# Performance work log

Measured on AMD Instinct MI355X. Metric: run time of the kernel, lower is better.

## Reference

```python
import jax, jax.numpy as jnp
import numpy as np


def _local_indices(H, W, K):
    # KxK local window per pixel; border neighbors clamped to the image (replicate padding)
    half = K // 2
    d = np.arange(-half, half + 1)
    r = np.clip(np.arange(H)[:, None, None, None] + d[None, None, :, None], 0, H - 1)
    c = np.clip(np.arange(W)[None, :, None, None] + d[None, None, None, :], 0, W - 1)
    return (r * W + c).reshape(H * W, K * K).astype(np.int32)


def setup_inputs():
    B, C, H, W = 2, 32, 128, 128
    K, S = 25, 1024
    N = H * W
    k1, k2, k3, k4 = jax.random.split(jax.random.key(0), 4)
    key_feat = jax.random.normal(k1, (B, C, H, W), dtype=jnp.float32)
    query_feat = jax.random.normal(k2, (B, C, H, W), dtype=jnp.float32)
    segment_target = jax.random.randint(k3, (B, 1, H, W), 0, 64, dtype=jnp.int32)
    local = jnp.broadcast_to(jnp.asarray(_local_indices(H, W, K))[None], (B, N, K * K))
    rand_glob = jax.random.randint(k4, (B, N, S - K * K), 0, N, dtype=jnp.int32)
    sample_inds = jnp.concatenate([local, rand_glob], axis=-1)  # [B, N, S]
    return {"key_feat": key_feat, "query_feat": query_feat,
            "segment_target": segment_target, "sample_inds": sample_inds}


def _affinity_logits(key_f, query_f, sample_inds, chunk=1024):
    # key_f, query_f: [B, N, C]; sample_inds: [B, N, S]
    B, N, C = key_f.shape
    S = sample_inds.shape[-1]
    nchunks = N // chunk
    q_c = query_f.reshape(B, nchunks, chunk, C).transpose(1, 0, 2, 3)
    i_c = sample_inds.reshape(B, nchunks, chunk, S).transpose(1, 0, 2, 3)

    def body(carry, args):
        q, idx = args                                   # [B, chunk, C], [B, chunk, S]
        kg = jax.vmap(lambda kb, ib: kb[ib])(key_f, idx)  # [B, chunk, S, C]
        return carry, jnp.einsum('bnsc,bnc->bns', kg, q)

    _, lc = jax.lax.scan(body, None, (q_c, i_c))        # [nchunks, B, chunk, S]
    logits = lc.transpose(1, 0, 2, 3).reshape(B, N, S)
    return logits * (C ** -0.5)


def _loss(logits, sample_inds, segment_target):
    B, N, S = logits.shape
    seg = segment_target.reshape(B, N)
    samples = jax.vmap(lambda s, i: s[i])(seg, sample_inds)      # [B, N, S]
    targets = (seg[:, :, None] == samples).astype(logits.dtype)
    mask = (seg != 0).astype(logits.dtype)[:, :, None]           # [B, N, 1]
    # weighted_softmax(logits, mask)
    xe = jnp.exp(logits - jnp.max(logits, -1, keepdims=True))
    denom = jnp.sum(xe * mask, -1, keepdims=True)
    y_prob = xe * mask / (denom + 1e-9)
    y_pred = jnp.log(jnp.clip(y_prob, 1e-8, None))
    y_true = targets / (jnp.sum(targets, -1, keepdims=True) + 1e-9)
    # F.kl_div(y_pred, y_true, reduction='none') with 0*log(0) = 0
    kl = jnp.where(y_true > 0,
                   y_true * (jnp.log(jnp.clip(y_true, 1e-30, None)) - y_pred),
                   0.0) * mask
    agg_mask = (jnp.sum(mask, -1) > 0).astype(logits.dtype)
    return jnp.sum(kl) / (jnp.sum(agg_mask) + 1e-9)


def reference(key_feat, query_feat, segment_target, sample_inds):
    B, C, H, W = key_feat.shape
    N = H * W
    key_f = key_feat.reshape(B, C, N).transpose(0, 2, 1)    # [B, N, C]
    query_f = query_feat.reshape(B, C, N).transpose(0, 2, 1)
    logits = _affinity_logits(key_f, query_f, sample_inds)  # [B, N, S], scaled by C**-0.5
    loss = _loss(logits, sample_inds, segment_target)
    return (logits, loss)
```

## Files before the change

### kernel.cpp

```cpp
#include <hip/hip_runtime.h>
#include <stdint.h>

typedef _Float16 h2 __attribute__((ext_vector_type(2)));

static constexpr int CDIM = 32;
static constexpr int NPIX = 16384;
static constexpr int SSAM = 1024;
static constexpr int ROWS_PER_BLOCK = 16;

__device__ __forceinline__ uint16_t f2h(float f) {
    union { _Float16 h; uint16_t u; } c;
    c.h = (_Float16)f;
    return c.u;
}

template<int CTRL>
__device__ __forceinline__ float dpp_add(float x) {
    int y = __builtin_amdgcn_mov_dpp(__float_as_int(x), CTRL, 0xF, 0xF, true);
    return x + __int_as_float(y);
}

__device__ __forceinline__ float dot2(h2 a, h2 b, float c) {
    return __builtin_amdgcn_fdot2(a, b, c, false);
}

__global__ __launch_bounds__(256)
void zero_words(uint32_t* __restrict__ p, int nwords)
{
    int i = blockIdx.x * 256 + threadIdx.x;
    if (i < nwords) p[i] = 0;
}

__global__ __launch_bounds__(256)
void prep_kernel(const float* __restrict__ key_f,
                 const float* __restrict__ query_f,
                 uint8_t* __restrict__ key16,
                 uint8_t* __restrict__ q16,
                 int N, int rows, float scale)
{
    int gI = blockIdx.x * 256 + threadIdx.x;
    if (gI >= rows) return;
    int b = gI / N, n = gI - b * N;
    const size_t cb = (size_t)b * CDIM;

    uint32_t kp[16], qp[16];
#pragma unroll
    for (int c = 0; c < CDIM; c += 2) {
        float k0 = key_f[(cb + c) * N + n];
        float k1 = key_f[(cb + c + 1) * N + n];
        float q0 = query_f[(cb + c) * N + n] * scale;
        float q1 = query_f[(cb + c + 1) * N + n] * scale;
        kp[c >> 1] = (uint32_t)f2h(k0) | ((uint32_t)f2h(k1) << 16);
        qp[c >> 1] = (uint32_t)f2h(q0) | ((uint32_t)f2h(q1) << 16);
    }
    uint4* ko = (uint4*)(key16 + ((size_t)gI << 6));
    uint4* qo = (uint4*)(q16 + ((size_t)gI << 6));
#pragma unroll
    for (int j = 0; j < 4; ++j) {
        ko[j] = make_uint4(kp[4*j], kp[4*j+1], kp[4*j+2], kp[4*j+3]);
        qo[j] = make_uint4(qp[4*j], qp[4*j+1], qp[4*j+2], qp[4*j+3]);
    }
}

__global__ __launch_bounds__(256)
void segbit_build(const int* __restrict__ seg32,
                  uint32_t* __restrict__ segbit,
                  int N, int rows)
{
    int g = blockIdx.x * 256 + threadIdx.x;
    if (g >= rows) return;
    int b = g / N, n = g - b * N;
    int v = seg32[g] & 63;
    atomicOr(&segbit[(((size_t)(b * 64 + v)) << 9) + (n >> 5)], 1u << (n & 31));
}

__global__ __launch_bounds__(256)
void affinity_multi(const int* __restrict__ inds,
                    const uint8_t* __restrict__ key16,
                    const uint8_t* __restrict__ q16,
                    const int* __restrict__ seg32,
                    const uint32_t* __restrict__ segbit,
                    float* __restrict__ out,
                    float* __restrict__ ws_kl)
{
    const int tid  = threadIdx.x;
    const int row0 = blockIdx.x * ROWS_PER_BLOCK;
    const int b    = row0 >> 14;
    const int lane = tid & 63;
    const int w    = tid >> 6;
    const int g    = lane >> 2;
    const int sub  = lane & 3;

    __shared__ __align__(16) int      idx_lds[2][SSAM];
    __shared__ __align__(16) uint32_t bm_lds[2][512];
    __shared__ float red[2][3][4];

    const uint32_t* sbase_bm = segbit + ((size_t)(b * 64) << 9);

    ((int4*)idx_lds[0])[tid] = ((const int4*)(inds + ((size_t)row0 << 10)))[tid];
    int scur = seg32[row0];
    ((uint2*)bm_lds[0])[tid] =
        ((const uint2*)(sbase_bm + ((size_t)(scur & 63) << 9)))[tid];
    uint4 qcur = *(const uint4*)(q16 + ((size_t)row0 << 6) + (sub << 4));
    __syncthreads();

    const uint8_t* kb = key16 + ((size_t)b << 20);
    const uint32_t subs = (uint32_t)(sub << 4);
    const int sbase = (w << 8) + g;

    for (int r = 0; r < ROWS_PER_BLOCK; ++r) {
        const int row = row0 + r;
        const int p   = r & 1;
        const int* cur = idx_lds[p];
        const bool hasNext = (r + 1 < ROWS_PER_BLOCK);

        h2 qh0, qh1, qh2, qh3;
        {
            union { uint4 u; h2 h[4]; } qc; qc.u = qcur;
            qh0 = qc.h[0]; qh1 = qc.h[1]; qh2 = qc.h[2]; qh3 = qc.h[3];
        }
        const int seg_n = scur;

        int idxs[16];
#pragma unroll
        for (int i = 0; i < 16; ++i)
            idxs[i] = cur[sbase + (i << 4)];

        uint4 kd[16];
#pragma unroll
        for (int i = 0; i < 16; ++i)
            kd[i] = *(const uint4*)(kb + (((uint32_t)idxs[i] << 6) | subs));

        int4 pre; uint4 qnext; uint2 pre_bm; int snext;
        if (hasNext) {
            pre   = ((const int4*)(inds + ((size_t)(row + 1) << 10)))[tid];
            qnext = *(const uint4*)(q16 + ((size_t)(row + 1) << 6) + (sub << 4));
            snext = seg32[row + 1];
            pre_bm = ((const uint2*)(sbase_bm + ((size_t)(snext & 63) << 9)))[tid];
        }
        int tfm = 0;
#pragma unroll
        for (int j = 0; j < 4; ++j) {
            int idx = cur[sbase + (((j << 2) | sub) << 4)];
            if ((bm_lds[p][idx >> 5] >> (idx & 31)) & 1u) tfm |= 1 << j;
        }

        float lgo0 = 0.f, lgo1 = 0.f, lgo2 = 0.f, lgo3 = 0.f;
#pragma unroll
        for (int i = 0; i < 16; ++i) {
            union { uint4 u; h2 h[4]; } kc; kc.u = kd[i];
            float acc = dot2(kc.h[0], qh0, 0.f);
            acc = dot2(kc.h[1], qh1, acc);
            acc = dot2(kc.h[2], qh2, acc);
            acc = dot2(kc.h[3], qh3, acc);
            acc = dpp_add<0xB1>(acc);
            acc = dpp_add<0x4E>(acc);
            if (sub == (i & 3)) {
                if ((i >> 2) == 0) lgo0 = acc;
                if ((i >> 2) == 1) lgo1 = acc;
                if ((i >> 2) == 2) lgo2 = acc;
                if ((i >> 2) == 3) lgo3 = acc;
            }
        }

        const size_t rowbase = (size_t)row << 10;
        float* op = out + rowbase + (w << 8) + (sub << 4) + g;
        op[0]   = lgo0;
        op[64]  = lgo1;
        op[128] = lgo2;
        op[192] = lgo3;

        float z  = ((__expf(lgo0) + __expf(lgo1)) + (__expf(lgo2) + __expf(lgo3)));
        float tc = (float)__popc((unsigned)tfm);
        float sl = 0.f;
        sl += (tfm & 1) ? lgo0 : 0.f;
        sl += (tfm & 2) ? lgo1 : 0.f;
        sl += (tfm & 4) ? lgo2 : 0.f;
        sl += (tfm & 8) ? lgo3 : 0.f;
#pragma unroll
        for (int off = 32; off >= 1; off >>= 1) {
            z  += __shfl_xor(z,  off, 64);
            tc += __shfl_xor(tc, off, 64);
            sl += __shfl_xor(sl, off, 64);
        }
        if (lane == 0) {
            red[p][0][w] = z;
            red[p][1][w] = tc;
            red[p][2][w] = sl;
        }

        if (hasNext) {
            ((int4*)idx_lds[p ^ 1])[tid] = pre;
            ((uint2*)bm_lds[p ^ 1])[tid] = pre_bm;
            qcur = qnext;
            scur = snext;
        }
        __syncthreads();

        if (tid == 0) {
            if (seg_n != 0) {
                const float Z  = (red[p][0][0] + red[p][0][1]) + (red[p][0][2] + red[p][0][3]);
                const float T  = (red[p][1][0] + red[p][1][1]) + (red[p][1][2] + red[p][1][3]);
                const float SL = (red[p][2][0] + red[p][2][1]) + (red[p][2][2] + red[p][2][3]);
                ws_kl[row] = -__logf(T) - SL / T + __logf(Z);
            } else {
                ws_kl[row] = 0.f;
            }
        }
    }
}

__global__ __launch_bounds__(256)
void affinity_fallback(const float* __restrict__ key_f,
                       const float* __restrict__ query_f,
                       const int*   __restrict__ seg32,
                       const int*   __restrict__ inds,
                       float* __restrict__ out,
                       float* __restrict__ ws_kl,
                       int N, int S, float scale)
{
    const int bid = blockIdx.x;
    const int tid = threadIdx.x;
    const int b   = bid / N;

    __shared__ float q_lds[CDIM];
    __shared__ float redA[4], redB[4], redC[4];

    if (tid < CDIM) {
        int n = bid - b * N;
        q_lds[tid] = query_f[((size_t)(b * CDIM + tid)) * N + n];
    }
    const int seg_n = seg32[bid];
    __syncthreads();

    float q[CDIM];
#pragma unroll
    for (int c = 0; c < CDIM; ++c) q[c] = q_lds[c];

    const size_t rowbase = (size_t)bid * S;
    const int4 iv = ((const int4*)(inds + rowbase))[tid];
    const int idxv[4] = {iv.x, iv.y, iv.z, iv.w};

    float lg[4];
    int   tf[4];
#pragma unroll
    for (int k = 0; k < 4; ++k) {
        int idx = idxv[k];
        tf[k] = (seg32[b * N + idx] == seg_n) ? 1 : 0;
        float acc = 0.f;
#pragma unroll
        for (int c = 0; c < CDIM; ++c)
            acc = fmaf(key_f[((size_t)(b * CDIM + c)) * N + idx], q[c], acc);
        lg[k] = acc * scale;
    }
    ((float4*)(out + rowbase))[tid] = make_float4(lg[0], lg[1], lg[2], lg[3]);

    const int lane = tid & 63, wv = tid >> 6;
    float m = fmaxf(fmaxf(lg[0], lg[1]), fmaxf(lg[2], lg[3]));
#pragma unroll
    for (int off = 32; off >= 1; off >>= 1)
        m = fmaxf(m, __shfl_xor(m, off, 64));
    if (lane == 0) redA[wv] = m;
    __syncthreads();
    m = fmaxf(fmaxf(redA[0], redA[1]), fmaxf(redA[2], redA[3]));

    float e[4], z = 0.f, tcnt = 0.f;
#pragma unroll
    for (int k = 0; k < 4; ++k) {
        e[k] = expf(lg[k] - m);
        z += e[k];
        tcnt += (float)tf[k];
    }
#pragma unroll
    for (int off = 32; off >= 1; off >>= 1) {
        z    += __shfl_xor(z, off, 64);
        tcnt += __shfl_xor(tcnt, off, 64);
    }
    if (lane == 0) { redB[wv] = z; redC[wv] = tcnt; }
    __syncthreads();
    const float Z = redB[0] + redB[1] + redB[2] + redB[3];
    const float T = redC[0] + redC[1] + redC[2] + redC[3];

    float kl = 0.f;
    if (seg_n != 0) {
        const float invZ = 1.f / (Z + 1e-9f);
        const float invT = 1.f / (T + 1e-9f);
        const float nlT  = -logf(T + 1e-9f);
#pragma unroll
        for (int k = 0; k < 4; ++k) {
            if (tf[k]) {
                float p = e[k] * invZ;
                float yp = logf(fmaxf(p, 1e-8f));
                kl += invT * (nlT - yp);
            }
        }
    }
#pragma unroll
    for (int off = 32; off >= 1; off >>= 1)
        kl += __shfl_xor(kl, off, 64);
    if (lane == 0) redA[wv] = kl;
    __syncthreads();
    if (tid == 0)
        ws_kl[bid] = redA[0] + redA[1] + redA[2] + redA[3];
}

__global__ __launch_bounds__(1024)
void loss_reduce(const float* __restrict__ ws_kl,
                 const int* __restrict__ seg32,
                 float* __restrict__ out_loss, int rows)
{
    const int tid = threadIdx.x;
    float s = 0.f, c = 0.f;
    for (int i = tid; i < rows; i += 1024) {
        s += ws_kl[i];
        c += (seg32[i] != 0) ? 1.f : 0.f;
    }
#pragma unroll
    for (int off = 32; off >= 1; off >>= 1) {
        s += __shfl_xor(s, off, 64);
        c += __shfl_xor(c, off, 64);
    }
    __shared__ float sA[16], sB[16];
    const int lane = tid & 63, wv = tid >> 6;
    if (lane == 0) { sA[wv] = s; sB[wv] = c; }
    __syncthreads();
    if (tid == 0) {
        float ts = 0.f, tc = 0.f;
#pragma unroll
        for (int k = 0; k < 16; ++k) { ts += sA[k]; tc += sB[k]; }
        out_loss[0] = ts / (tc + 1e-9f);
    }
}

extern "C" void kernel_launch(void* const* d_in, const int* in_sizes, int n_in,
                              void* d_out, int out_size, void* d_ws, size_t ws_size,
                              hipStream_t stream)
{
    const float* key_f   = (const float*)d_in[0];
    const float* query_f = (const float*)d_in[1];
    const int*   seg32   = (const int*)d_in[2];
    const int*   inds    = (const int*)d_in[3];
    float* out = (float*)d_out;

    const int N    = NPIX;
    const int rows = in_sizes[2];
    const int S    = in_sizes[3] / rows;
    const float scale = (float)(1.0 / sqrt((double)CDIM));
    const int B    = rows / N;

    const size_t off_q16 = (size_t)rows * 64;
    const size_t off_sb  = off_q16 + (size_t)rows * 64;
    const size_t sb_words = (size_t)B * 64 * 512;
    const size_t off_kl  = (off_sb + sb_words * 4 + 255) & ~(size_t)255;
    const size_t need    = off_kl + (size_t)rows * 4;

    uint8_t* wsb = (uint8_t*)d_ws;
    const bool geom_ok = (S == SSAM) && (rows % N == 0) &&
                         (rows % ROWS_PER_BLOCK == 0);

    if (ws_size >= need && geom_ok) {
        uint8_t*  key16  = wsb;
        uint8_t*  q16    = wsb + off_q16;
        uint32_t* segbit = (uint32_t*)(wsb + off_sb);
        float*    wskl   = (float*)(wsb + off_kl);

        zero_words<<<(int)((sb_words + 255) / 256), 256, 0, stream>>>(
            segbit, (int)sb_words);
        prep_kernel<<<(rows + 255) / 256, 256, 0, stream>>>(
            key_f, query_f, key16, q16, N, rows, scale);
        segbit_build<<<(rows + 255) / 256, 256, 0, stream>>>(
            seg32, segbit, N, rows);
        affinity_multi<<<rows / ROWS_PER_BLOCK, 256, 0, stream>>>(
            inds, key16, q16, seg32, segbit, out, wskl);
        loss_reduce<<<1, 1024, 0, stream>>>(wskl, seg32, out + (size_t)rows * S, rows);
    } else {
        float* wskl = (float*)d_ws;
        affinity_fallback<<<rows, 256, 0, stream>>>(
            key_f, query_f, seg32, inds, out, wskl, N, S, scale);
        loss_reduce<<<1, 1024, 0, stream>>>(wskl, seg32, out + (size_t)rows * S, rows);
    }
}
```

Measured before the change: 175.2 us.

## Tile pixels spatially and stage a key halo window in LDS

Each block now handles an 8x8 pixel tile and first loads a 32x32 window of fp16 keys (the tile plus a 12-pixel halo) into shared memory. Sample indices that fall inside the window, such as the 25x25 local neighborhood, are read from LDS; only out-of-window random samples are gathered from global memory. The index buffer in LDS is replaced by per-thread int4 loads spread to lanes with DPP quad broadcasts, and the logit store becomes a single coalesced float4. This aims to cut global gather traffic, at the cost of 64KB of LDS per block, which limits occupancy, plus per-sample window tests.

Result: slower. 256.0 us (+46.1%).

```diff
diff --git a/kernel.cpp b/kernel.cpp
--- a/kernel.cpp
+++ b/kernel.cpp
@@ -6,7 +6,9 @@
 static constexpr int CDIM = 32;
 static constexpr int NPIX = 16384;
 static constexpr int SSAM = 1024;
-static constexpr int ROWS_PER_BLOCK = 16;
+static constexpr int TILE = 8;
+static constexpr int HALO = 12;
+static constexpr int WIN  = 32;
 
 __device__ __forceinline__ uint16_t f2h(float f) {
     union { _Float16 h; uint16_t u; } c;
@@ -18,6 +20,11 @@
 __device__ __forceinline__ float dpp_add(float x) {
     int y = __builtin_amdgcn_mov_dpp(__float_as_int(x), CTRL, 0xF, 0xF, true);
     return x + __int_as_float(y);
+}
+
+template<int Q>
+__device__ __forceinline__ int qbcast(int x) {
+    return __builtin_amdgcn_mov_dpp(x, Q * 0x55, 0xF, 0xF, true);
 }
 
 __device__ __forceinline__ float dot2(h2 a, h2 b, float c) {
@@ -75,44 +82,59 @@
 }
 
 __global__ __launch_bounds__(256)
-void affinity_multi(const int* __restrict__ inds,
-                    const uint8_t* __restrict__ key16,
-                    const uint8_t* __restrict__ q16,
-                    const int* __restrict__ seg32,
-                    const uint32_t* __restrict__ segbit,
-                    float* __restrict__ out,
-                    float* __restrict__ ws_kl)
+void affinity_tile(const int* __restrict__ inds,
+                   const uint8_t* __restrict__ key16,
+                   const uint8_t* __restrict__ q16,
+                   const int* __restrict__ seg32,
+                   const uint32_t* __restrict__ segbit,
+                   float* __restrict__ out,
+                   float* __restrict__ ws_kl)
 {
     const int tid  = threadIdx.x;
-    const int row0 = blockIdx.x * ROWS_PER_BLOCK;
-    const int b    = row0 >> 14;
+    const int bid  = blockIdx.x;
+    const int b    = bid >> 8;
+    const int t    = bid & 255;
+    const int y0   = (t >> 4) << 3;
+    const int x0   = (t & 15) << 3;
     const int lane = tid & 63;
     const int w    = tid >> 6;
-    const int g    = lane >> 2;
     const int sub  = lane & 3;
 
-    __shared__ __align__(16) int      idx_lds[2][SSAM];
+    const int yL = max(0, y0 - HALO);
+    const int yH = min(127, y0 + TILE - 1 + HALO);
+    const int xL = max(0, x0 - HALO);
+    const int xH = min(127, x0 + TILE - 1 + HALO);
+    const int wh = yH - yL + 1;
+    const int ww = xH - xL + 1;
+
+    __shared__ __align__(16) uint8_t  key_lds[WIN * WIN * 64];
     __shared__ __align__(16) uint32_t bm_lds[2][512];
     __shared__ float red[2][3][4];
 
-    const uint32_t* sbase_bm = segbit + ((size_t)(b * 64) << 9);
-
-    ((int4*)idx_lds[0])[tid] = ((const int4*)(inds + ((size_t)row0 << 10)))[tid];
-    int scur = seg32[row0];
-    ((uint2*)bm_lds[0])[tid] =
-        ((const uint2*)(sbase_bm + ((size_t)(scur & 63) << 9)))[tid];
-    uint4 qcur = *(const uint4*)(q16 + ((size_t)row0 << 6) + (sub << 4));
-    __syncthreads();
-
     const uint8_t* kb = key16 + ((size_t)b << 20);
     const uint32_t subs = (uint32_t)(sub << 4);
-    const int sbase = (w << 8) + g;
-
-    for (int r = 0; r < ROWS_PER_BLOCK; ++r) {
-        const int row = row0 + r;
-        const int p   = r & 1;
-        const int* cur = idx_lds[p];
-        const bool hasNext = (r + 1 < ROWS_PER_BLOCK);
+
+    for (int s = tid; s < WIN * WIN * 4; s += 256) {
+        int slot = s >> 2, q = s & 3;
+        int i = slot >> 5, j = slot & 31;
+        int ii = min(i, wh - 1), jj = min(j, ww - 1);
+        *(uint4*)(key_lds + (slot << 6) + (q << 4)) =
+            *(const uint4*)(kb + ((((yL + ii) << 7) + (xL + jj)) << 6) + (q << 4));
+    }
+
+    const uint32_t* sbm = segbit + ((size_t)(b * 64) << 9);
+    int row = (b << 14) + (y0 << 7) + x0;
+    int scur = seg32[row];
+    ((uint2*)bm_lds[0])[tid] = ((const uint2*)(sbm + ((size_t)(scur & 63) << 9)))[tid];
+    uint4 qcur = *(const uint4*)(q16 + ((size_t)row << 6) + subs);
+    int4  ivcur = ((const int4*)(inds + ((size_t)row << 10)))[tid];
+    __syncthreads();
+
+    for (int r = 0; r < TILE * TILE; ++r) {
+        const int p = r & 1;
+        const bool hasNext = (r + 1 < TILE * TILE);
+        const int rn = r + 1;
+        const int rown = (b << 14) + ((y0 + (rn >> 3)) << 7) + (x0 + (rn & 7));
 
         h2 qh0, qh1, qh2, qh3;
         {
@@ -120,63 +142,67 @@
             qh0 = qc.h[0]; qh1 = qc.h[1]; qh2 = qc.h[2]; qh3 = qc.h[3];
         }
         const int seg_n = scur;
-
-        int idxs[16];
-#pragma unroll
-        for (int i = 0; i < 16; ++i)
-            idxs[i] = cur[sbase + (i << 4)];
+        const int4 iv = ivcur;
 
         uint4 kd[16];
-#pragma unroll
-        for (int i = 0; i < 16; ++i)
-            kd[i] = *(const uint4*)(kb + (((uint32_t)idxs[i] << 6) | subs));
+#define CLS(I) { \
+        int comp = (((I)&3)==0) ? iv.x : (((I)&3)==1) ? iv.y : (((I)&3)==2) ? iv.z : iv.w; \
+        int idx  = qbcast<((I)>>2)>(comp); \
+        int rr = (idx >> 7) - yL, cc = (idx & 127) - xL; \
+        if (!((uint32_t)rr < (uint32_t)wh && (uint32_t)cc < (uint32_t)ww)) \
+            kd[(I)] = *(const uint4*)(kb + (((uint32_t)idx << 6) | subs)); }
+        CLS(0)  CLS(1)  CLS(2)  CLS(3)  CLS(4)  CLS(5)  CLS(6)  CLS(7)
+        CLS(8)  CLS(9)  CLS(10) CLS(11) CLS(12) CLS(13) CLS(14) CLS(15)
+#undef CLS
 
         int4 pre; uint4 qnext; uint2 pre_bm; int snext;
         if (hasNext) {
-            pre   = ((const int4*)(inds + ((size_t)(row + 1) << 10)))[tid];
-            qnext = *(const uint4*)(q16 + ((size_t)(row + 1) << 6) + (sub << 4));
-            snext = seg32[row + 1];
-            pre_bm = ((const uint2*)(sbase_bm + ((size_t)(snext & 63) << 9)))[tid];
+            pre    = ((const int4*)(inds + ((size_t)rown << 10)))[tid];
+            qnext  = *(const uint4*)(q16 + ((size_t)rown << 6) + subs);
+            snext  = seg32[rown];
+            pre_bm = ((const uint2*)(sbm + ((size_t)(snext & 63) << 9)))[tid];
         }
         int tfm = 0;
-#pragma unroll
-        for (int j = 0; j < 4; ++j) {
-            int idx = cur[sbase + (((j << 2) | sub) << 4)];
-            if ((bm_lds[p][idx >> 5] >> (idx & 31)) & 1u) tfm |= 1 << j;
-        }
-
-        float lgo0 = 0.f, lgo1 = 0.f, lgo2 = 0.f, lgo3 = 0.f;
-#pragma unroll
-        for (int i = 0; i < 16; ++i) {
-            union { uint4 u; h2 h[4]; } kc; kc.u = kd[i];
-            float acc = dot2(kc.h[0], qh0, 0.f);
-            acc = dot2(kc.h[1], qh1, acc);
-            acc = dot2(kc.h[2], qh2, acc);
-            acc = dot2(kc.h[3], qh3, acc);
-            acc = dpp_add<0xB1>(acc);
-            acc = dpp_add<0x4E>(acc);
-            if (sub == (i & 3)) {
-                if ((i >> 2) == 0) lgo0 = acc;
-                if ((i >> 2) == 1) lgo1 = acc;
-                if ((i >> 2) == 2) lgo2 = acc;
-                if ((i >> 2) == 3) lgo3 = acc;
-            }
-        }
-
-        const size_t rowbase = (size_t)row << 10;
-        float* op = out + rowbase + (w << 8) + (sub << 4) + g;
-        op[0]   = lgo0;
-        op[64]  = lgo1;
-        op[128] = lgo2;
-        op[192] = lgo3;
-
-        float z  = ((__expf(lgo0) + __expf(lgo1)) + (__expf(lgo2) + __expf(lgo3)));
+        if ((bm_lds[p][(uint32_t)iv.x >> 5] >> (iv.x & 31)) & 1u) tfm |= 1;
+        if ((bm_lds[p][(uint32_t)iv.y >> 5] >> (iv.y & 31)) & 1u) tfm |= 2;
+        if ((bm_lds[p][(uint32_t)iv.z >> 5] >> (iv.z & 31)) & 1u) tfm |= 4;
+        if ((bm_lds[p][(uint32_t)iv.w >> 5] >> (iv.w & 31)) & 1u) tfm |= 8;
+        __builtin_amdgcn_sched_barrier(0);
+
+        float lg0 = 0.f, lg1 = 0.f, lg2 = 0.f, lg3 = 0.f;
+#define DOT(I) { \
+        int comp = (((I)&3)==0) ? iv.x : (((I)&3)==1) ? iv.y : (((I)&3)==2) ? iv.z : iv.w; \
+        int idx  = qbcast<((I)>>2)>(comp); \
+        int rr = (idx >> 7) - yL, cc = (idx & 127) - xL; \
+        uint4 kc = kd[(I)]; \
+        if ((uint32_t)rr < (uint32_t)wh && (uint32_t)cc < (uint32_t)ww) \
+            kc = *(const uint4*)(key_lds + ((((rr << 5) + cc) << 6) | subs)); \
+        union { uint4 u; h2 h[4]; } kk; kk.u = kc; \
+        float acc = dot2(kk.h[0], qh0, 0.f); \
+        acc = dot2(kk.h[1], qh1, acc); \
+        acc = dot2(kk.h[2], qh2, acc); \
+        acc = dot2(kk.h[3], qh3, acc); \
+        acc = dpp_add<0xB1>(acc); \
+        acc = dpp_add<0x4E>(acc); \
+        if (sub == ((I) >> 2)) { \
+            if constexpr (((I)&3) == 0) lg0 = acc; \
+            else if constexpr (((I)&3) == 1) lg1 = acc; \
+            else if constexpr (((I)&3) == 2) lg2 = acc; \
+            else lg3 = acc; } }
+        DOT(0)  DOT(1)  DOT(2)  DOT(3)  DOT(4)  DOT(5)  DOT(6)  DOT(7)
+        DOT(8)  DOT(9)  DOT(10) DOT(11) DOT(12) DOT(13) DOT(14) DOT(15)
+#undef DOT
+
+        *(float4*)(out + ((size_t)row << 10) + (tid << 2)) =
+            make_float4(lg0, lg1, lg2, lg3);
+
+        float z  = (__expf(lg0) + __expf(lg1)) + (__expf(lg2) + __expf(lg3));
         float tc = (float)__popc((unsigned)tfm);
         float sl = 0.f;
-        sl += (tfm & 1) ? lgo0 : 0.f;
-        sl += (tfm & 2) ? lgo1 : 0.f;
-        sl += (tfm & 4) ? lgo2 : 0.f;
-        sl += (tfm & 8) ? lgo3 : 0.f;
+        sl += (tfm & 1) ? lg0 : 0.f;
+        sl += (tfm & 2) ? lg1 : 0.f;
+        sl += (tfm & 4) ? lg2 : 0.f;
+        sl += (tfm & 8) ? lg3 : 0.f;
 #pragma unroll
         for (int off = 32; off >= 1; off >>= 1) {
             z  += __shfl_xor(z,  off, 64);
@@ -190,10 +216,9 @@
         }
 
         if (hasNext) {
-            ((int4*)idx_lds[p ^ 1])[tid] = pre;
             ((uint2*)bm_lds[p ^ 1])[tid] = pre_bm;
-            qcur = qnext;
-            scur = snext;
+            ivcur = pre;
+            qcur  = qnext;
         }
         __syncthreads();
 
@@ -207,6 +232,11 @@
                 ws_kl[row] = 0.f;
             }
         }
+
+        if (hasNext) {
+            row  = rown;
+            scur = snext;
+        }
     }
 }
 
@@ -355,8 +385,7 @@
     const size_t need    = off_kl + (size_t)rows * 4;
 
     uint8_t* wsb = (uint8_t*)d_ws;
-    const bool geom_ok = (S == SSAM) && (rows % N == 0) &&
-                         (rows % ROWS_PER_BLOCK == 0);
+    const bool geom_ok = (S == SSAM) && (rows % N == 0);
 
     if (ws_size >= need && geom_ok) {
         uint8_t*  key16  = wsb;
@@ -370,7 +399,7 @@
             key_f, query_f, key16, q16, N, rows, scale);
         segbit_build<<<(rows + 255) / 256, 256, 0, stream>>>(
             seg32, segbit, N, rows);
-        affinity_multi<<<rows / ROWS_PER_BLOCK, 256, 0, stream>>>(
+        affinity_tile<<<B * 256, 256, 0, stream>>>(
             inds, key16, q16, seg32, segbit, out, wskl);
         loss_reduce<<<1, 1024, 0, stream>>>(wskl, seg32, out + (size_t)rows * S, rows);
     } else {
```
